# Optimization experiments

Measured on AMD Instinct MI355X. Metric: run time of the kernel, lower is better.

## Reference

```python
import jax, jax.numpy as jnp
import numpy as np

B, M, D, W = 4, 4096, 64, 128  # batch/heads, seq (m=n), head dim (k), nnz per row


def setup_inputs() -> dict:
    key = jax.random.key(0)
    kq, kk, kv, kc = jax.random.split(key, 4)
    q = jax.random.normal(kq, (B, M, D), dtype=jnp.float32)
    k = jax.random.normal(kk, (B, M, D), dtype=jnp.float32)
    v = jax.random.normal(kv, (B, M, D), dtype=jnp.float32)
    # CSR with uniform W nonzeros per row: row_offsets = arange(M+1)*W implicit,
    # column_indices flattened is [M*W]; stored here as [M, W].
    column_indices = jax.random.randint(kc, (M, W), 0, M).astype(jnp.int32)
    return {"q": q, "k": k, "v": v, "column_indices": column_indices}


def reference(q, k, v, column_indices):
    # SDDMM: logits[b,i,w] = <q[b,i,:], k[b, col[i,w], :]> at sparse positions only
    k_g = k[:, column_indices, :]                      # [B, M, W, D]
    logits = jnp.einsum('bmd,bmwd->bmw', q, k_g)       # sparse values per row
    # Sparse row-wise softmax (each CSR row has exactly W entries)
    weights = jax.nn.softmax(logits, axis=-1)          # [B, M, W]
    # SpMM: out[b,i,d] = sum_w weights[b,i,w] * v[b, col[i,w], d]
    v_g = v[:, column_indices, :]                      # [B, M, W, D]
    out = jnp.einsum('bmw,bmwd->bmd', weights, v_g)    # [B, M, D]
    return out
```

## Files before the change

kernel.cpp:

```cpp
#include <hip/hip_runtime.h>
#include <hip/hip_fp16.h>
#include <math.h>

constexpr int B = 4;
constexpr int M = 4096;
constexpr int D = 64;
constexpr int W = 128;
constexpr int NELEM = B * M * D;

__global__ __launch_bounds__(256) void cvt_f32_f16(const float4* __restrict__ src,
                                                   __half2* __restrict__ dst, int n4) {
    int i = blockIdx.x * 256 + threadIdx.x;
    if (i < n4) {
        float4 f = src[i];
        dst[2 * i]     = __floats2half2_rn(f.x, f.y);
        dst[2 * i + 1] = __floats2half2_rn(f.z, f.w);
    }
}

__global__ __launch_bounds__(128, 8) void sparse_attn_f16(
    const float* __restrict__ q,
    const __half* __restrict__ kh,
    const __half* __restrict__ vh,
    const int*   __restrict__ idx,
    float*       __restrict__ out)
{
    const int blk = blockIdx.x;
    const int b = blk & 3;
    const int m = blk >> 2;
    const int t = threadIdx.x;
    const int lane = t & 63;
    const int wave = t >> 6;
    const int ci = lane & 7;
    const int r  = lane >> 3;

    __shared__ int    idx_s[W];
    __shared__ float  sc_s[W];
    __shared__ float  red_s[4];
    __shared__ float4 opart4[16];

    idx_s[t] = idx[m * W + t];
    const float4* qrow = (const float4*)(q + ((size_t)b * M + m) * D);
    const float4 qa = qrow[2 * ci];
    const float4 qb = qrow[2 * ci + 1];
    __syncthreads();

    const __half* kb = kh + (size_t)b * M * D;
    const __half* vb = vh + (size_t)b * M * D;
    const int wbase = wave * 64;

    float4 kreg[8];
    #pragma unroll
    for (int j = 0; j < 8; ++j) {
        const int w = wbase + j * 8 + r;
        kreg[j] = ((const float4*)(kb + (size_t)idx_s[w] * D))[ci];
    }
    #pragma unroll
    for (int j = 0; j < 8; ++j) {
        const int w = wbase + j * 8 + r;
        const __half2* h = (const __half2*)&kreg[j];
        float2 f0 = __half22float2(h[0]);
        float2 f1 = __half22float2(h[1]);
        float2 f2 = __half22float2(h[2]);
        float2 f3 = __half22float2(h[3]);
        float part = f0.x * qa.x + f0.y * qa.y + f1.x * qa.z + f1.y * qa.w
                   + f2.x * qb.x + f2.y * qb.y + f3.x * qb.z + f3.y * qb.w;
        part += __shfl_xor(part, 1);
        part += __shfl_xor(part, 2);
        part += __shfl_xor(part, 4);
        if (ci == 0) sc_s[w] = part;
    }
    __syncthreads();

    float logit = sc_s[t];
    float mx = logit;
    #pragma unroll
    for (int o = 1; o < 64; o <<= 1) mx = fmaxf(mx, __shfl_xor(mx, o));
    if (lane == 0) red_s[wave] = mx;
    __syncthreads();
    mx = fmaxf(red_s[0], red_s[1]);
    float e = __expf(logit - mx);
    float sm = e;
    #pragma unroll
    for (int o = 1; o < 64; o <<= 1) sm += __shfl_xor(sm, o);
    if (lane == 0) red_s[2 + wave] = sm;
    __syncthreads();
    const float inv = 1.0f / (red_s[2] + red_s[3]);
    sc_s[t] = e * inv;
    __syncthreads();

    float4 vreg[8];
    #pragma unroll
    for (int j = 0; j < 8; ++j) {
        const int w = wbase + j * 8 + r;
        vreg[j] = ((const float4*)(vb + (size_t)idx_s[w] * D))[ci];
    }
    float acc[8] = {0, 0, 0, 0, 0, 0, 0, 0};
    #pragma unroll
    for (int j = 0; j < 8; ++j) {
        const int w = wbase + j * 8 + r;
        const float p = sc_s[w];
        const __half2* h = (const __half2*)&vreg[j];
        #pragma unroll
        for (int c = 0; c < 4; ++c) {
            float2 f = __half22float2(h[c]);
            acc[2 * c]     += p * f.x;
            acc[2 * c + 1] += p * f.y;
        }
    }
    #pragma unroll
    for (int o = 8; o < 64; o <<= 1) {
        #pragma unroll
        for (int i = 0; i < 8; ++i) acc[i] += __shfl_xor(acc[i], o);
    }
    if (wave == 0 && r == 0) {
        opart4[2 * ci]     = make_float4(acc[0], acc[1], acc[2], acc[3]);
        opart4[2 * ci + 1] = make_float4(acc[4], acc[5], acc[6], acc[7]);
    }
    __syncthreads();
    if (wave == 1 && r == 0) {
        float4 o0 = opart4[2 * ci];
        float4 o1 = opart4[2 * ci + 1];
        float4* orow = (float4*)(out + ((size_t)b * M + m) * D);
        orow[2 * ci]     = make_float4(o0.x + acc[0], o0.y + acc[1],
                                       o0.z + acc[2], o0.w + acc[3]);
        orow[2 * ci + 1] = make_float4(o1.x + acc[4], o1.y + acc[5],
                                       o1.z + acc[6], o1.w + acc[7]);
    }
}

__global__ __launch_bounds__(128) void sparse_attn_f32(
    const float* __restrict__ q,
    const float* __restrict__ k,
    const float* __restrict__ v,
    const int*   __restrict__ idx,
    float*       __restrict__ out)
{
    const int blk = blockIdx.x;
    const int b = blk & 3;
    const int m = blk >> 2;
    const int t = threadIdx.x;
    const int lane = t & 63;
    const int wave = t >> 6;
    const int ci = lane & 15;
    const int r  = lane >> 4;

    __shared__ int   idx_s[W];
    __shared__ float sc_s[W];
    __shared__ float red_s[4];
    __shared__ float4 opart_s[16];

    idx_s[t] = idx[m * W + t];
    const float4 qf = ((const float4*)(q + ((size_t)b * M + m) * D))[ci];
    __syncthreads();

    const float* kb = k + (size_t)b * M * D;
    const int wbase = wave * 64;

    #pragma unroll
    for (int j = 0; j < 16; ++j) {
        const int w = wbase + j * 4 + r;
        const float4 kv = ((const float4*)(kb + (size_t)idx_s[w] * D))[ci];
        float part = kv.x * qf.x + kv.y * qf.y + kv.z * qf.z + kv.w * qf.w;
        part += __shfl_xor(part, 1);
        part += __shfl_xor(part, 2);
        part += __shfl_xor(part, 4);
        part += __shfl_xor(part, 8);
        if (ci == 0) sc_s[w] = part;
    }
    __syncthreads();

    float logit = sc_s[t];
    float mx = logit;
    #pragma unroll
    for (int o = 1; o < 64; o <<= 1) mx = fmaxf(mx, __shfl_xor(mx, o));
    if (lane == 0) red_s[wave] = mx;
    __syncthreads();
    mx = fmaxf(red_s[0], red_s[1]);
    float e = __expf(logit - mx);
    float sm = e;
    #pragma unroll
    for (int o = 1; o < 64; o <<= 1) sm += __shfl_xor(sm, o);
    if (lane == 0) red_s[2 + wave] = sm;
    __syncthreads();
    const float inv_denom = 1.0f / (red_s[2] + red_s[3]);
    sc_s[t] = e * inv_denom;
    __syncthreads();

    const float* vb = v + (size_t)b * M * D;
    float4 acc = {0.f, 0.f, 0.f, 0.f};
    #pragma unroll
    for (int j = 0; j < 16; ++j) {
        const int w = wbase + j * 4 + r;
        const float p = sc_s[w];
        const float4 vv = ((const float4*)(vb + (size_t)idx_s[w] * D))[ci];
        acc.x += p * vv.x; acc.y += p * vv.y;
        acc.z += p * vv.z; acc.w += p * vv.w;
    }
    acc.x += __shfl_xor(acc.x, 16); acc.y += __shfl_xor(acc.y, 16);
    acc.z += __shfl_xor(acc.z, 16); acc.w += __shfl_xor(acc.w, 16);
    acc.x += __shfl_xor(acc.x, 32); acc.y += __shfl_xor(acc.y, 32);
    acc.z += __shfl_xor(acc.z, 32); acc.w += __shfl_xor(acc.w, 32);

    if (wave == 0 && r == 0) opart_s[ci] = acc;
    __syncthreads();
    if (wave == 1 && r == 0) {
        const float4 o0 = opart_s[ci];
        float4 res;
        res.x = o0.x + acc.x; res.y = o0.y + acc.y;
        res.z = o0.z + acc.z; res.w = o0.w + acc.w;
        ((float4*)(out + ((size_t)b * M + m) * D))[ci] = res;
    }
}

extern "C" void kernel_launch(void* const* d_in, const int* in_sizes, int n_in,
                              void* d_out, int out_size, void* d_ws, size_t ws_size,
                              hipStream_t stream) {
    const float* q = (const float*)d_in[0];
    const float* k = (const float*)d_in[1];
    const float* v = (const float*)d_in[2];
    const int* idx = (const int*)d_in[3];
    float* out = (float*)d_out;

    const size_t need = (size_t)2 * NELEM * sizeof(__half);
    if (ws_size >= need) {
        __half* kh = (__half*)d_ws;
        __half* vh = kh + NELEM;
        const int n4 = NELEM / 4;
        const int cblk = (n4 + 255) / 256;
        cvt_f32_f16<<<cblk, 256, 0, stream>>>((const float4*)k, (__half2*)kh, n4);
        cvt_f32_f16<<<cblk, 256, 0, stream>>>((const float4*)v, (__half2*)vh, n4);
        sparse_attn_f16<<<B * M, 128, 0, stream>>>(q, kh, vh, idx, out);
    } else {
        sparse_attn_f32<<<B * M, 128, 0, stream>>>(q, k, v, idx, out);
    }
}
```

Before: 100.7 us.

## Map one wave per row, drop shared-memory softmax, fuse K/V conversion launches

The attention kernel now handles four query rows per 256-thread block, one row per wave. Each lane keeps its 16 logits in registers, so the softmax reduces with wave shuffles only. This removes the shared-memory score buffer and most block barriers, and normalisation is deferred to the final output scale. The two fp16 conversion launches are merged into one. The cost is more registers per thread (offsets, logits) and a smaller grid of larger blocks, which may reduce occupancy.

```diff
diff --git a/kernel.cpp b/kernel.cpp
--- a/kernel.cpp
+++ b/kernel.cpp
@@ -8,104 +8,112 @@
 constexpr int W = 128;
 constexpr int NELEM = B * M * D;
 
-__global__ __launch_bounds__(256) void cvt_f32_f16(const float4* __restrict__ src,
-                                                   __half2* __restrict__ dst, int n4) {
+__global__ __launch_bounds__(256) void cvt_f32_f16_2(
+    const float4* __restrict__ k, const float4* __restrict__ v,
+    __half2* __restrict__ kh, __half2* __restrict__ vh, int n4) {
     int i = blockIdx.x * 256 + threadIdx.x;
-    if (i < n4) {
-        float4 f = src[i];
-        dst[2 * i]     = __floats2half2_rn(f.x, f.y);
-        dst[2 * i + 1] = __floats2half2_rn(f.z, f.w);
-    }
-}
-
-__global__ __launch_bounds__(128, 8) void sparse_attn_f16(
+    const float4* src;
+    __half2* dst;
+    if (i < n4) { src = k; dst = kh; }
+    else        { src = v; dst = vh; i -= n4; if (i >= n4) return; }
+    float4 f = src[i];
+    dst[2 * i]     = __floats2half2_rn(f.x, f.y);
+    dst[2 * i + 1] = __floats2half2_rn(f.z, f.w);
+}
+
+__global__ __launch_bounds__(256, 4) void sparse_attn_f16(
     const float* __restrict__ q,
     const __half* __restrict__ kh,
     const __half* __restrict__ vh,
     const int*   __restrict__ idx,
     float*       __restrict__ out)
 {
-    const int blk = blockIdx.x;
-    const int b = blk & 3;
-    const int m = blk >> 2;
-    const int t = threadIdx.x;
+    const int blk  = blockIdx.x;
+    const int b    = blk & 3;
+    const int mb   = (blk >> 2) * 4;
+    const int t    = threadIdx.x;
+    const int wave = t >> 6;
     const int lane = t & 63;
-    const int wave = t >> 6;
-    const int ci = lane & 7;
-    const int r  = lane >> 3;
-
-    __shared__ int    idx_s[W];
-    __shared__ float  sc_s[W];
-    __shared__ float  red_s[4];
-    __shared__ float4 opart4[16];
-
-    idx_s[t] = idx[m * W + t];
-    const float4* qrow = (const float4*)(q + ((size_t)b * M + m) * D);
-    const float4 qa = qrow[2 * ci];
-    const float4 qb = qrow[2 * ci + 1];
-    __syncthreads();
+    const int ci   = lane & 7;
+    const int r    = lane >> 3;
+    const int m    = mb + wave;
+
+    __shared__ int idx_s[4 * W];
+
+    ((int2*)idx_s)[t] = ((const int2*)(idx + (size_t)mb * W))[t];
+
+    const float* qrow = q + ((size_t)b * M + m) * D;
+    const float4 qa = ((const float4*)qrow)[2 * ci];
+    const float4 qb = ((const float4*)qrow)[2 * ci + 1];
+
+    __syncthreads();
+
+    int off[16];
+    #pragma unroll
+    for (int j = 0; j < 16; ++j) off[j] = idx_s[wave * W + j * 8 + r];
 
     const __half* kb = kh + (size_t)b * M * D;
     const __half* vb = vh + (size_t)b * M * D;
-    const int wbase = wave * 64;
-
-    float4 kreg[8];
-    #pragma unroll
-    for (int j = 0; j < 8; ++j) {
-        const int w = wbase + j * 8 + r;
-        kreg[j] = ((const float4*)(kb + (size_t)idx_s[w] * D))[ci];
-    }
-    #pragma unroll
-    for (int j = 0; j < 8; ++j) {
-        const int w = wbase + j * 8 + r;
-        const __half2* h = (const __half2*)&kreg[j];
-        float2 f0 = __half22float2(h[0]);
-        float2 f1 = __half22float2(h[1]);
-        float2 f2 = __half22float2(h[2]);
-        float2 f3 = __half22float2(h[3]);
-        float part = f0.x * qa.x + f0.y * qa.y + f1.x * qa.z + f1.y * qa.w
-                   + f2.x * qb.x + f2.y * qb.y + f3.x * qb.z + f3.y * qb.w;
-        part += __shfl_xor(part, 1);
-        part += __shfl_xor(part, 2);
-        part += __shfl_xor(part, 4);
-        if (ci == 0) sc_s[w] = part;
-    }
-    __syncthreads();
-
-    float logit = sc_s[t];
-    float mx = logit;
-    #pragma unroll
-    for (int o = 1; o < 64; o <<= 1) mx = fmaxf(mx, __shfl_xor(mx, o));
-    if (lane == 0) red_s[wave] = mx;
-    __syncthreads();
-    mx = fmaxf(red_s[0], red_s[1]);
-    float e = __expf(logit - mx);
-    float sm = e;
-    #pragma unroll
-    for (int o = 1; o < 64; o <<= 1) sm += __shfl_xor(sm, o);
-    if (lane == 0) red_s[2 + wave] = sm;
-    __syncthreads();
-    const float inv = 1.0f / (red_s[2] + red_s[3]);
-    sc_s[t] = e * inv;
-    __syncthreads();
-
-    float4 vreg[8];
-    #pragma unroll
-    for (int j = 0; j < 8; ++j) {
-        const int w = wbase + j * 8 + r;
-        vreg[j] = ((const float4*)(vb + (size_t)idx_s[w] * D))[ci];
-    }
+
+    float larr[16];
+    #pragma unroll
+    for (int batch = 0; batch < 2; ++batch) {
+        float4 kreg[8];
+        #pragma unroll
+        for (int jj = 0; jj < 8; ++jj) {
+            const int j = batch * 8 + jj;
+            kreg[jj] = *(const float4*)(kb + (size_t)off[j] * D + ci * 8);
+        }
+        #pragma unroll
+        for (int jj = 0; jj < 8; ++jj) {
+            const __half2* h = (const __half2*)&kreg[jj];
+            float2 f0 = __half22float2(h[0]);
+            float2 f1 = __half22float2(h[1]);
+            float2 f2 = __half22float2(h[2]);
+            float2 f3 = __half22float2(h[3]);
+            float part = f0.x * qa.x + f0.y * qa.y + f1.x * qa.z + f1.y * qa.w
+                       + f2.x * qb.x + f2.y * qb.y + f3.x * qb.z + f3.y * qb.w;
+            part += __shfl_xor(part, 1);
+            part += __shfl_xor(part, 2);
+            part += __shfl_xor(part, 4);
+            larr[batch * 8 + jj] = part;
+        }
+    }
+
+    float mx = larr[0];
+    #pragma unroll
+    for (int j = 1; j < 16; ++j) mx = fmaxf(mx, larr[j]);
+    mx = fmaxf(mx, __shfl_xor(mx, 8));
+    mx = fmaxf(mx, __shfl_xor(mx, 16));
+    mx = fmaxf(mx, __shfl_xor(mx, 32));
+
+    float sum = 0.f;
+    #pragma unroll
+    for (int j = 0; j < 16; ++j) { larr[j] = __expf(larr[j] - mx); sum += larr[j]; }
+    sum += __shfl_xor(sum, 8);
+    sum += __shfl_xor(sum, 16);
+    sum += __shfl_xor(sum, 32);
+    const float inv = 1.0f / sum;
+
     float acc[8] = {0, 0, 0, 0, 0, 0, 0, 0};
     #pragma unroll
-    for (int j = 0; j < 8; ++j) {
-        const int w = wbase + j * 8 + r;
-        const float p = sc_s[w];
-        const __half2* h = (const __half2*)&vreg[j];
-        #pragma unroll
-        for (int c = 0; c < 4; ++c) {
-            float2 f = __half22float2(h[c]);
-            acc[2 * c]     += p * f.x;
-            acc[2 * c + 1] += p * f.y;
+    for (int batch = 0; batch < 2; ++batch) {
+        float4 vreg[8];
+        #pragma unroll
+        for (int jj = 0; jj < 8; ++jj) {
+            const int j = batch * 8 + jj;
+            vreg[jj] = *(const float4*)(vb + (size_t)off[j] * D + ci * 8);
+        }
+        #pragma unroll
+        for (int jj = 0; jj < 8; ++jj) {
+            const float p = larr[batch * 8 + jj];
+            const __half2* h = (const __half2*)&vreg[jj];
+            #pragma unroll
+            for (int c = 0; c < 4; ++c) {
+                float2 f = __half22float2(h[c]);
+                acc[2 * c]     += p * f.x;
+                acc[2 * c + 1] += p * f.y;
+            }
         }
     }
     #pragma unroll
@@ -113,19 +121,13 @@
         #pragma unroll
         for (int i = 0; i < 8; ++i) acc[i] += __shfl_xor(acc[i], o);
     }
-    if (wave == 0 && r == 0) {
-        opart4[2 * ci]     = make_float4(acc[0], acc[1], acc[2], acc[3]);
-        opart4[2 * ci + 1] = make_float4(acc[4], acc[5], acc[6], acc[7]);
-    }
-    __syncthreads();
-    if (wave == 1 && r == 0) {
-        float4 o0 = opart4[2 * ci];
-        float4 o1 = opart4[2 * ci + 1];
+
+    if (r == 0) {
         float4* orow = (float4*)(out + ((size_t)b * M + m) * D);
-        orow[2 * ci]     = make_float4(o0.x + acc[0], o0.y + acc[1],
-                                       o0.z + acc[2], o0.w + acc[3]);
-        orow[2 * ci + 1] = make_float4(o1.x + acc[4], o1.y + acc[5],
-                                       o1.z + acc[6], o1.w + acc[7]);
+        orow[2 * ci]     = make_float4(acc[0] * inv, acc[1] * inv,
+                                       acc[2] * inv, acc[3] * inv);
+        orow[2 * ci + 1] = make_float4(acc[4] * inv, acc[5] * inv,
+                                       acc[6] * inv, acc[7] * inv);
     }
 }
 
@@ -227,10 +229,10 @@
         __half* kh = (__half*)d_ws;
         __half* vh = kh + NELEM;
         const int n4 = NELEM / 4;
-        const int cblk = (n4 + 255) / 256;
-        cvt_f32_f16<<<cblk, 256, 0, stream>>>((const float4*)k, (__half2*)kh, n4);
-        cvt_f32_f16<<<cblk, 256, 0, stream>>>((const float4*)v, (__half2*)vh, n4);
-        sparse_attn_f16<<<B * M, 128, 0, stream>>>(q, kh, vh, idx, out);
+        const int cblk = (2 * n4 + 255) / 256;
+        cvt_f32_f16_2<<<cblk, 256, 0, stream>>>((const float4*)k, (const float4*)v,
+                                                (__half2*)kh, (__half2*)vh, n4);
+        sparse_attn_f16<<<B * M / 4, 256, 0, stream>>>(q, kh, vh, idx, out);
     } else {
         sparse_attn_f32<<<B * M, 128, 0, stream>>>(q, k, v, idx, out);
     }
```

Result: faster. 95.99 us (-4.7%).
